# Performance work log

Measured on AMD Instinct MI355X. Metric: run time of the kernel, lower is better.

## Reference

```python
import jax, jax.numpy as jnp
import numpy as np

B, SQ, SKV, D, H = 4, 2048, 2048, 1024, 16
DH = D // H  # 64


def setup_inputs() -> dict:
    key = jax.random.key(0)
    ks = jax.random.split(key, 8)
    s = 0.02  # realistic init scale for weights
    return {
        "query": jax.random.normal(ks[0], (B, SQ, D), dtype=jnp.float32),
        "value": jax.random.normal(ks[1], (B, SKV, D), dtype=jnp.float32),
        "wq": jax.random.normal(ks[2], (H, D, DH), dtype=jnp.float32) * s,
        "bq": jnp.zeros((H, DH), dtype=jnp.float32),
        "wk": jax.random.normal(ks[3], (H, D, DH), dtype=jnp.float32) * s,
        "bk": jnp.zeros((H, DH), dtype=jnp.float32),
        "wv": jax.random.normal(ks[4], (H, D, DH), dtype=jnp.float32) * s,
        "bv": jnp.zeros((H, DH), dtype=jnp.float32),
        "wo": jax.random.normal(ks[5], (D, D), dtype=jnp.float32) * s,
        "bo": jnp.zeros((D,), dtype=jnp.float32),
    }


def reference(query, value, wq, bq, wk, bk, wv, bv, wo, bo):
    # Batched equivalent of the per-head Dense loop: [B,S,D] x [H,D,DH] -> [B,H,S,DH]
    q = jnp.einsum("bsd,hde->bhse", query, wq) + bq[None, :, None, :]
    k = jnp.einsum("bsd,hde->bhse", value, wk) + bk[None, :, None, :]
    v = jnp.einsum("bsd,hde->bhse", value, wv) + bv[None, :, None, :]
    scale = 1.0 / jnp.sqrt(jnp.asarray(DH, dtype=q.dtype))
    scores = jnp.einsum("bhqe,bhke->bhqk", q, k) * scale  # [B,H,SQ,SKV]
    align = jax.nn.softmax(scores, axis=-1)
    heads = jnp.einsum("bhqk,bhke->bhqe", align, v)  # [B,H,SQ,DH]
    # concat heads along feature dim (head order preserved)
    heads = jnp.transpose(heads, (0, 2, 1, 3)).reshape(B, SQ, D)
    return heads @ wo + bo
```

## Files before the change

### kernel.cpp

```cpp
#include <hip/hip_runtime.h>
#include <stdint.h>

#define DEVI __device__ __forceinline__

typedef __bf16  bf16x8 __attribute__((ext_vector_type(8)));
typedef float   f32x4  __attribute__((ext_vector_type(4)));
typedef float   f32x16 __attribute__((ext_vector_type(16)));
typedef uint32_t u32x4 __attribute__((ext_vector_type(4)));
typedef uint32_t u32x2v __attribute__((ext_vector_type(2)));
typedef uint16_t u16x8 __attribute__((ext_vector_type(8)));
typedef uint16_t u16x4 __attribute__((ext_vector_type(4)));

static constexpr int BB = 4, SQL = 2048, SKVL = 2048, DMODEL = 1024, NH = 16;
static constexpr int MROWS = BB * SQL;
static constexpr int KD = DMODEL;

DEVI uint16_t f2bf(float x) {
  uint32_t u = __builtin_bit_cast(uint32_t, x);
  u += 0x7FFFu + ((u >> 16) & 1u);
  return (uint16_t)(u >> 16);
}
DEVI uint32_t cvt2bf(float a, float b) {
  __bf16 x = (__bf16)a, y = (__bf16)b;
  return (uint32_t)__builtin_bit_cast(uint16_t, x) |
         ((uint32_t)__builtin_bit_cast(uint16_t, y) << 16);
}
DEVI f32x4 mfma16(bf16x8 a, bf16x8 b, f32x4 c) {
  return __builtin_amdgcn_mfma_f32_16x16x32_bf16(a, b, c, 0, 0, 0);
}
DEVI f32x16 mfma32(bf16x8 a, bf16x8 b, f32x16 c) {
  return __builtin_amdgcn_mfma_f32_32x32x16_bf16(a, b, c, 0, 0, 0);
}
DEVI void gload16(const void* g, void* l) {
  __builtin_amdgcn_global_load_lds((__attribute__((address_space(1))) const void*)g,
                                   (__attribute__((address_space(3))) void*)l, 16, 0, 0);
}
DEVI bf16x8 ldread(const void* p) { return __builtin_bit_cast(bf16x8, *(const u32x4*)p); }
DEVI u32x2v plswap(uint32_t a, uint32_t b) {
  return __builtin_amdgcn_permlane32_swap(a, b, false, false);
}

__global__ __launch_bounds__(256) void k_cvt_act(const float* __restrict__ q, const float* __restrict__ v,
                                                 uint16_t* __restrict__ aq, uint16_t* __restrict__ av) {
  const int64_t n4 = (int64_t)MROWS * DMODEL / 4;
  for (int64_t i = (int64_t)blockIdx.x * 256 + threadIdx.x; i < 2 * n4; i += (int64_t)gridDim.x * 256) {
    const bool second = (i >= n4);
    const int64_t j = second ? i - n4 : i;
    const float4 x = (second ? (const float4*)v : (const float4*)q)[j];
    u16x4 o = { f2bf(x.x), f2bf(x.y), f2bf(x.z), f2bf(x.w) };
    *(u16x4*)((second ? av : aq) + j * 4) = o;
  }
}

__global__ __launch_bounds__(256) void k_cvt_w(const float* __restrict__ wq, const float* __restrict__ wk,
                                               const float* __restrict__ wv, const float* __restrict__ wo,
                                               uint16_t* __restrict__ wt) {
  const int idx = blockIdx.x * 256 + threadIdx.x;
  const int z = idx >> 20, f = idx & 1048575;
  const int n = f >> 10, d = f & 1023;
  const float* w = (z == 0) ? wq : (z == 1) ? wk : (z == 2) ? wv : wo;
  const float x = (z < 3) ? w[((n >> 6) << 16) + d * 64 + (n & 63)] : w[d * 1024 + n];
  wt[(size_t)z * 1048576 + f] = f2bf(x);
}

template <int MODE>
__global__ __launch_bounds__(256) void k_gemm(const uint16_t* __restrict__ A, const uint16_t* __restrict__ Bt,
                                              const float* __restrict__ bias, const float* __restrict__ biasB,
                                              void* __restrict__ outp, void* __restrict__ outpB,
                                              float oscale) {
  __shared__ __align__(16) uint16_t Al[128 * 64];
  __shared__ __align__(16) uint16_t Bl[128 * 64];
  const int tid = threadIdx.x;
  const int w = tid >> 6, ln = tid & 63;
  const int g = ln >> 4, lc = ln & 15;
  const int m0 = blockIdx.x * 128, n0 = blockIdx.y * 128;
  const int wm = (w >> 1) * 64, wn = (w & 1) * 64;
  const int srow = w * 32 + (ln >> 3);
  const int colp = (ln & 7) * 16;

  f32x4 acc[4][4] = {};

  for (int kt = 0; kt < KD / 64; ++kt) {
    #pragma unroll
    for (int i = 0; i < 4; ++i) {
      const int row = srow + i * 8;
      const int colb = colp ^ ((row & 7) << 4);
      gload16((const char*)(A + (size_t)(m0 + row) * KD + kt * 64) + colb,
              (char*)Al + w * 4096 + i * 1024);
      gload16((const char*)(Bt + (size_t)(n0 + row) * KD + kt * 64) + colb,
              (char*)Bl + w * 4096 + i * 1024);
    }
    __syncthreads();
    #pragma unroll
    for (int kk = 0; kk < 2; ++kk) {
      bf16x8 af[4], bfr[4];
      #pragma unroll
      for (int mt = 0; mt < 4; ++mt) {
        const int row = wm + mt * 16 + lc;
        af[mt] = ldread((const char*)Al + row * 128 + ((kk * 64 + g * 16) ^ ((row & 7) << 4)));
      }
      #pragma unroll
      for (int nt = 0; nt < 4; ++nt) {
        const int row = wn + nt * 16 + lc;
        bfr[nt] = ldread((const char*)Bl + row * 128 + ((kk * 64 + g * 16) ^ ((row & 7) << 4)));
      }
      #pragma unroll
      for (int mt = 0; mt < 4; ++mt)
        #pragma unroll
        for (int nt = 0; nt < 4; ++nt)
          acc[mt][nt] = mfma16(af[mt], bfr[nt], acc[mt][nt]);
    }
    __syncthreads();
  }
  #pragma unroll
  for (int nt = 0; nt < 4; ++nt) {
    const int n = n0 + wn + nt * 16 + lc;
    const int z = (MODE == 2) ? (n >> 10) : 0;
    const int nn = (MODE == 2) ? (n & 1023) : n;
    const float bv = (MODE == 2) ? (z ? biasB : bias)[nn] : bias[n];
    uint16_t* dst16 = (uint16_t*)((MODE == 2 && z) ? outpB : outp);
    #pragma unroll
    for (int mt = 0; mt < 4; ++mt) {
      #pragma unroll
      for (int r = 0; r < 4; ++r) {
        const int m = m0 + wm + mt * 16 + g * 4 + r;
        if (MODE != 1) {
          float val = acc[mt][nt][r] + bv;
          if (MODE == 0) val *= oscale;
          const int b = m >> 11, s = m & 2047, h = nn >> 6, e = nn & 63;
          dst16[((size_t)((b * NH + h) * SQL + s)) * 64 + e] = f2bf(val);
        } else {
          ((float*)outp)[(size_t)m * DMODEL + n] = acc[mt][nt][r] + bv;
        }
      }
    }
  }
}

__global__ __launch_bounds__(512, 4) void k_attn(const uint16_t* __restrict__ Qb,
                                                 const uint16_t* __restrict__ Kb,
                                                 const uint16_t* __restrict__ Vb,
                                                 uint16_t* __restrict__ Hd) {
  __shared__ __align__(16) uint16_t Kl[2][64 * 64];
  __shared__ __align__(16) uint16_t Vl[2][64 * 64];
  const int tid = threadIdx.x;
  const int w = tid >> 6, ln = tid & 63;
  const int ql = ln & 31, hi = ln >> 5;
  const int bh = blockIdx.y;
  const int q0 = blockIdx.x * 256 + w * 32;

  const uint16_t* Qp = Qb + ((size_t)bh * SQL + q0 + ql) * 64;
  bf16x8 qf[4];
  #pragma unroll
  for (int s = 0; s < 4; ++s)
    qf[s] = __builtin_bit_cast(bf16x8, *(const u16x8*)(Qp + s * 16 + hi * 8));

  const uint16_t* Kbase = Kb + (size_t)bh * SKVL * 64;
  const uint16_t* Vbase = Vb + (size_t)bh * SKVL * 64;

  const int swl = (ln & 7) << 4;
  const int e0off = (hi << 4) ^ swl;
  const int rb = ql * 128;

  const bool kstage = (w < 4);
  const int krow0 = (w & 3) * 16 + (ln >> 3);
  const int kcolb = (((ln & 7) ^ (ln >> 3)) << 4);
  const int t2 = tid & 255;
  const int vkv = (t2 & 31) * 2, ve0 = (t2 >> 5) * 8;

  f32x16 acc0 = {}, acc1 = {};
  float lsum = 0.f;

  if (kstage) {
    #pragma unroll
    for (int i = 0; i < 2; ++i) {
      const int row = krow0 + i * 8;
      gload16((const char*)(Kbase + (size_t)row * 64) + kcolb,
              (char*)&Kl[0][0] + (w & 3) * 2048 + i * 1024);
    }
  } else {
    const u16x8 a = *(const u16x8*)(Vbase + (size_t)vkv * 64 + ve0);
    const u16x8 b = *(const u16x8*)(Vbase + (size_t)(vkv + 1) * 64 + ve0);
    #pragma unroll
    for (int i = 0; i < 8; ++i) {
      const int e = ve0 + i;
      *(uint32_t*)((char*)&Vl[0][0] + e * 128 + ((vkv * 2) ^ ((e & 7) << 4))) =
          (uint32_t)a[i] | ((uint32_t)b[i] << 16);
    }
  }
  __syncthreads();

  int cur = 0;
  for (int t = 0; t < SKVL / 64; ++t) {
    const bool pre = (t + 1 < SKVL / 64);
    u16x8 nv0, nv1;
    if (pre) {
      if (kstage) {
        const uint16_t* Kc = Kbase + (size_t)(t + 1) * 4096;
        #pragma unroll
        for (int i = 0; i < 2; ++i) {
          const int row = krow0 + i * 8;
          gload16((const char*)(Kc + (size_t)row * 64) + kcolb,
                  (char*)&Kl[cur ^ 1][0] + (w & 3) * 2048 + i * 1024);
        }
      } else {
        const uint16_t* Vc = Vbase + (size_t)(t + 1) * 4096;
        nv0 = *(const u16x8*)(Vc + (size_t)vkv * 64 + ve0);
        nv1 = *(const u16x8*)(Vc + (size_t)(vkv + 1) * 64 + ve0);
      }
    }
    const char* Kc0 = (const char*)&Kl[cur][0];
    f32x16 s0 = {}, s1 = {};
    __builtin_amdgcn_s_setprio(1);
    #pragma unroll
    for (int s = 0; s < 4; ++s) {
      const int off = e0off ^ (s << 5);
      const bf16x8 k0 = ldread(Kc0 + rb + off);
      const bf16x8 k1 = ldread(Kc0 + 4096 + rb + off);
      s0 = mfma32(k0, qf[s], s0);
      s1 = mfma32(k1, qf[s], s1);
    }
    __builtin_amdgcn_s_setprio(0);
    float ps = 0.f;
    #pragma unroll
    for (int r = 0; r < 16; ++r) {
      s0[r] = __builtin_amdgcn_exp2f(s0[r]);
      s1[r] = __builtin_amdgcn_exp2f(s1[r]);
      ps += s0[r] + s1[r];
    }
    lsum += ps;
    uint32_t w32[2][4][2];
    #pragma unroll
    for (int c8 = 0; c8 < 4; ++c8) {
      #pragma unroll
      for (int p = 0; p < 2; ++p) {
        w32[0][c8][p] = cvt2bf(s0[4 * c8 + 2 * p], s0[4 * c8 + 2 * p + 1]);
        w32[1][c8][p] = cvt2bf(s1[4 * c8 + 2 * p], s1[4 * c8 + 2 * p + 1]);
      }
    }
    const char* Vc0 = (const char*)&Vl[cur][0];
    __builtin_amdgcn_s_setprio(1);
    #pragma unroll
    for (int u = 0; u < 4; ++u) {
      const int tt = u >> 1, ul = u & 1;
      const u32x2v e0 = plswap(w32[tt][2 * ul][0], w32[tt][2 * ul + 1][0]);
      const u32x2v e1 = plswap(w32[tt][2 * ul][1], w32[tt][2 * ul + 1][1]);
      u32x4 pj;
      pj[0] = e0[0]; pj[1] = e1[0]; pj[2] = e0[1]; pj[3] = e1[1];
      const bf16x8 pb = __builtin_bit_cast(bf16x8, pj);
      const int off = e0off ^ (u << 5);
      const bf16x8 v0 = ldread(Vc0 + rb + off);
      const bf16x8 v1 = ldread(Vc0 + 4096 + rb + off);
      acc0 = mfma32(v0, pb, acc0);
      acc1 = mfma32(v1, pb, acc1);
    }
    __builtin_amdgcn_s_setprio(0);
    if (pre && !kstage) {
      #pragma unroll
      for (int i = 0; i < 8; ++i) {
        const int e = ve0 + i;
        *(uint32_t*)((char*)&Vl[cur ^ 1][0] + e * 128 + ((vkv * 2) ^ ((e & 7) << 4))) =
            (uint32_t)nv0[i] | ((uint32_t)nv1[i] << 16);
      }
    }
    __syncthreads();
    cur ^= 1;
  }
  const float lt = lsum + __shfl_xor(lsum, 32);
  const float inv = __builtin_amdgcn_rcpf(lt);
  const int b = bh >> 4, h = bh & 15;
  uint16_t* op = Hd + ((size_t)(b * SQL + q0 + ql)) * DMODEL + h * 64;
  #pragma unroll
  for (int et = 0; et < 2; ++et) {
    #pragma unroll
    for (int r2 = 0; r2 < 8; ++r2) {
      const float v0 = (et ? acc1[2 * r2] : acc0[2 * r2]) * inv;
      const float v1 = (et ? acc1[2 * r2 + 1] : acc0[2 * r2 + 1]) * inv;
      const int e = et * 32 + 4 * hi + (r2 & 1) * 2 + (r2 >> 1) * 8;
      *(uint32_t*)(op + e) = cvt2bf(v0, v1);
    }
  }
}

extern "C" void kernel_launch(void* const* d_in, const int* in_sizes, int n_in,
                              void* d_out, int out_size, void* d_ws, size_t ws_size,
                              hipStream_t stream) {
  const float* query = (const float*)d_in[0];
  const float* value = (const float*)d_in[1];
  const float* wq = (const float*)d_in[2];
  const float* bq = (const float*)d_in[3];
  const float* wk = (const float*)d_in[4];
  const float* bk = (const float*)d_in[5];
  const float* wv = (const float*)d_in[6];
  const float* bv = (const float*)d_in[7];
  const float* wo = (const float*)d_in[8];
  const float* bo = (const float*)d_in[9];

  const size_t SZ_ACT = (size_t)MROWS * DMODEL * 2;
  const size_t SZ_W   = (size_t)4 * DMODEL * DMODEL * 2;
  if (ws_size < 6 * SZ_ACT + SZ_W) return;

  char* ws = (char*)d_ws;
  uint16_t* Aq = (uint16_t*)ws;  ws += SZ_ACT;
  uint16_t* Av = (uint16_t*)ws;  ws += SZ_ACT;
  uint16_t* Wt = (uint16_t*)ws;  ws += SZ_W;
  uint16_t* Qb = (uint16_t*)ws;  ws += SZ_ACT;
  uint16_t* Kb = (uint16_t*)ws;  ws += SZ_ACT;
  uint16_t* Vb = (uint16_t*)ws;  ws += SZ_ACT;
  uint16_t* Hd = (uint16_t*)ws;  ws += SZ_ACT;

  const float QSCALE = 0.18033688011112042f;

  k_cvt_act<<<dim3(2048), dim3(256), 0, stream>>>(query, value, Aq, Av);
  k_cvt_w<<<dim3(16384), dim3(256), 0, stream>>>(wq, wk, wv, wo, Wt);
  k_gemm<0><<<dim3(64, 8), dim3(256), 0, stream>>>(Aq, Wt, bq, nullptr, Qb, nullptr, QSCALE);
  k_gemm<2><<<dim3(64, 16), dim3(256), 0, stream>>>(Av, Wt + 1048576, bk, bv, Kb, Vb, 1.0f);
  k_attn<<<dim3(8, 64), dim3(512), 0, stream>>>(Qb, Kb, Vb, Hd);
  k_gemm<1><<<dim3(64, 8), dim3(256), 0, stream>>>(Hd, Wt + 3145728, bo, nullptr, d_out, nullptr, 1.0f);
}
```

Measured before the change: 219.8 us.

## Double-buffer GEMM LDS, fuse conversion kernels, reshape attention blocks with XCD swizzle

Merges the activation and weight bf16 conversion kernels into a single launch. Adds LDS double buffering to the GEMM so the next K tile loads while MFMAs run on the current one, with one barrier per iteration instead of two. Reshapes the attention kernel from 512-thread blocks with specialised K and V loader warps into 256-thread blocks where every warp stages both K and V. It also remaps the 1D grid so consecutive blocks spread across XCDs. The GEMM doubles its LDS use and the attention change alters occupancy and per-warp load work.

```diff
diff --git a/kernel.cpp b/kernel.cpp
--- a/kernel.cpp
+++ b/kernel.cpp
@@ -40,27 +40,29 @@
   return __builtin_amdgcn_permlane32_swap(a, b, false, false);
 }
 
-__global__ __launch_bounds__(256) void k_cvt_act(const float* __restrict__ q, const float* __restrict__ v,
-                                                 uint16_t* __restrict__ aq, uint16_t* __restrict__ av) {
-  const int64_t n4 = (int64_t)MROWS * DMODEL / 4;
-  for (int64_t i = (int64_t)blockIdx.x * 256 + threadIdx.x; i < 2 * n4; i += (int64_t)gridDim.x * 256) {
-    const bool second = (i >= n4);
-    const int64_t j = second ? i - n4 : i;
-    const float4 x = (second ? (const float4*)v : (const float4*)q)[j];
-    u16x4 o = { f2bf(x.x), f2bf(x.y), f2bf(x.z), f2bf(x.w) };
-    *(u16x4*)((second ? av : aq) + j * 4) = o;
-  }
-}
-
-__global__ __launch_bounds__(256) void k_cvt_w(const float* __restrict__ wq, const float* __restrict__ wk,
-                                               const float* __restrict__ wv, const float* __restrict__ wo,
-                                               uint16_t* __restrict__ wt) {
-  const int idx = blockIdx.x * 256 + threadIdx.x;
-  const int z = idx >> 20, f = idx & 1048575;
-  const int n = f >> 10, d = f & 1023;
-  const float* w = (z == 0) ? wq : (z == 1) ? wk : (z == 2) ? wv : wo;
-  const float x = (z < 3) ? w[((n >> 6) << 16) + d * 64 + (n & 63)] : w[d * 1024 + n];
-  wt[(size_t)z * 1048576 + f] = f2bf(x);
+__global__ __launch_bounds__(256) void k_cvt(const float* __restrict__ q, const float* __restrict__ v,
+                                             const float* __restrict__ wq, const float* __restrict__ wk,
+                                             const float* __restrict__ wv, const float* __restrict__ wo,
+                                             uint16_t* __restrict__ aq, uint16_t* __restrict__ av,
+                                             uint16_t* __restrict__ wt) {
+  const int bx = blockIdx.x;
+  if (bx < 16384) {
+    const int idx = bx * 256 + threadIdx.x;
+    const int z = idx >> 20, f = idx & 1048575;
+    const int n = f >> 10, d = f & 1023;
+    const float* w = (z == 0) ? wq : (z == 1) ? wk : (z == 2) ? wv : wo;
+    const float x = (z < 3) ? w[((n >> 6) << 16) + d * 64 + (n & 63)] : w[d * 1024 + n];
+    wt[(size_t)z * 1048576 + f] = f2bf(x);
+  } else {
+    const int64_t n4 = (int64_t)MROWS * DMODEL / 4;
+    for (int64_t i = (int64_t)(bx - 16384) * 256 + threadIdx.x; i < 2 * n4; i += (int64_t)2048 * 256) {
+      const bool second = (i >= n4);
+      const int64_t j = second ? i - n4 : i;
+      const float4 x = (second ? (const float4*)v : (const float4*)q)[j];
+      u16x4 o = { f2bf(x.x), f2bf(x.y), f2bf(x.z), f2bf(x.w) };
+      *(u16x4*)((second ? av : aq) + j * 4) = o;
+    }
+  }
 }
 
 template <int MODE>
@@ -68,8 +70,8 @@
                                               const float* __restrict__ bias, const float* __restrict__ biasB,
                                               void* __restrict__ outp, void* __restrict__ outpB,
                                               float oscale) {
-  __shared__ __align__(16) uint16_t Al[128 * 64];
-  __shared__ __align__(16) uint16_t Bl[128 * 64];
+  __shared__ __align__(16) uint16_t Al[2][128 * 64];
+  __shared__ __align__(16) uint16_t Bl[2][128 * 64];
   const int tid = threadIdx.x;
   const int w = tid >> 6, ln = tid & 63;
   const int g = ln >> 4, lc = ln & 15;
@@ -80,29 +82,41 @@
 
   f32x4 acc[4][4] = {};
 
-  for (int kt = 0; kt < KD / 64; ++kt) {
+  auto stage = [&](int kt, int bs) {
     #pragma unroll
     for (int i = 0; i < 4; ++i) {
       const int row = srow + i * 8;
       const int colb = colp ^ ((row & 7) << 4);
       gload16((const char*)(A + (size_t)(m0 + row) * KD + kt * 64) + colb,
-              (char*)Al + w * 4096 + i * 1024);
+              (char*)&Al[bs][0] + w * 4096 + i * 1024);
       gload16((const char*)(Bt + (size_t)(n0 + row) * KD + kt * 64) + colb,
-              (char*)Bl + w * 4096 + i * 1024);
-    }
-    __syncthreads();
+              (char*)&Bl[bs][0] + w * 4096 + i * 1024);
+    }
+  };
+
+  stage(0, 0);
+  asm volatile("s_waitcnt vmcnt(0)" ::: "memory");
+  __builtin_amdgcn_s_barrier();
+  __builtin_amdgcn_sched_barrier(0);
+
+  int cur = 0;
+  #pragma unroll 2
+  for (int kt = 0; kt < KD / 64; ++kt) {
+    if (kt + 1 < KD / 64) stage(kt + 1, cur ^ 1);
+    const char* Ac = (const char*)&Al[cur][0];
+    const char* Bc = (const char*)&Bl[cur][0];
     #pragma unroll
     for (int kk = 0; kk < 2; ++kk) {
       bf16x8 af[4], bfr[4];
       #pragma unroll
       for (int mt = 0; mt < 4; ++mt) {
         const int row = wm + mt * 16 + lc;
-        af[mt] = ldread((const char*)Al + row * 128 + ((kk * 64 + g * 16) ^ ((row & 7) << 4)));
+        af[mt] = ldread(Ac + row * 128 + ((kk * 64 + g * 16) ^ ((row & 7) << 4)));
       }
       #pragma unroll
       for (int nt = 0; nt < 4; ++nt) {
         const int row = wn + nt * 16 + lc;
-        bfr[nt] = ldread((const char*)Bl + row * 128 + ((kk * 64 + g * 16) ^ ((row & 7) << 4)));
+        bfr[nt] = ldread(Bc + row * 128 + ((kk * 64 + g * 16) ^ ((row & 7) << 4)));
       }
       #pragma unroll
       for (int mt = 0; mt < 4; ++mt)
@@ -110,8 +124,12 @@
         for (int nt = 0; nt < 4; ++nt)
           acc[mt][nt] = mfma16(af[mt], bfr[nt], acc[mt][nt]);
     }
-    __syncthreads();
-  }
+    asm volatile("s_waitcnt vmcnt(0)" ::: "memory");
+    __builtin_amdgcn_s_barrier();
+    __builtin_amdgcn_sched_barrier(0);
+    cur ^= 1;
+  }
+
   #pragma unroll
   for (int nt = 0; nt < 4; ++nt) {
     const int n = n0 + wn + nt * 16 + lc;
@@ -137,7 +155,7 @@
   }
 }
 
-__global__ __launch_bounds__(512, 4) void k_attn(const uint16_t* __restrict__ Qb,
+__global__ __launch_bounds__(256, 3) void k_attn(const uint16_t* __restrict__ Qb,
                                                  const uint16_t* __restrict__ Kb,
                                                  const uint16_t* __restrict__ Vb,
                                                  uint16_t* __restrict__ Hd) {
@@ -146,8 +164,10 @@
   const int tid = threadIdx.x;
   const int w = tid >> 6, ln = tid & 63;
   const int ql = ln & 31, hi = ln >> 5;
-  const int bh = blockIdx.y;
-  const int q0 = blockIdx.x * 256 + w * 32;
+  const int bsw = blockIdx.x;
+  const int l = (bsw & 7) * 128 + (bsw >> 3);
+  const int qx = l & 15, bh = l >> 4;
+  const int q0 = qx * 128 + w * 32;
 
   const uint16_t* Qp = Qb + ((size_t)bh * SQL + q0 + ql) * 64;
   bf16x8 qf[4];
@@ -162,23 +182,20 @@
   const int e0off = (hi << 4) ^ swl;
   const int rb = ql * 128;
 
-  const bool kstage = (w < 4);
-  const int krow0 = (w & 3) * 16 + (ln >> 3);
+  const int krow0 = w * 16 + (ln >> 3);
   const int kcolb = (((ln & 7) ^ (ln >> 3)) << 4);
-  const int t2 = tid & 255;
-  const int vkv = (t2 & 31) * 2, ve0 = (t2 >> 5) * 8;
+  const int vkv = (tid & 31) * 2, ve0 = (tid >> 5) * 8;
 
   f32x16 acc0 = {}, acc1 = {};
   float lsum = 0.f;
 
-  if (kstage) {
+  {
     #pragma unroll
     for (int i = 0; i < 2; ++i) {
       const int row = krow0 + i * 8;
       gload16((const char*)(Kbase + (size_t)row * 64) + kcolb,
-              (char*)&Kl[0][0] + (w & 3) * 2048 + i * 1024);
-    }
-  } else {
+              (char*)&Kl[0][0] + w * 2048 + i * 1024);
+    }
     const u16x8 a = *(const u16x8*)(Vbase + (size_t)vkv * 64 + ve0);
     const u16x8 b = *(const u16x8*)(Vbase + (size_t)(vkv + 1) * 64 + ve0);
     #pragma unroll
@@ -195,19 +212,16 @@
     const bool pre = (t + 1 < SKVL / 64);
     u16x8 nv0, nv1;
     if (pre) {
-      if (kstage) {
-        const uint16_t* Kc = Kbase + (size_t)(t + 1) * 4096;
-        #pragma unroll
-        for (int i = 0; i < 2; ++i) {
-          const int row = krow0 + i * 8;
-          gload16((const char*)(Kc + (size_t)row * 64) + kcolb,
-                  (char*)&Kl[cur ^ 1][0] + (w & 3) * 2048 + i * 1024);
-        }
-      } else {
-        const uint16_t* Vc = Vbase + (size_t)(t + 1) * 4096;
-        nv0 = *(const u16x8*)(Vc + (size_t)vkv * 64 + ve0);
-        nv1 = *(const u16x8*)(Vc + (size_t)(vkv + 1) * 64 + ve0);
-      }
+      const uint16_t* Kc = Kbase + (size_t)(t + 1) * 4096;
+      #pragma unroll
+      for (int i = 0; i < 2; ++i) {
+        const int row = krow0 + i * 8;
+        gload16((const char*)(Kc + (size_t)row * 64) + kcolb,
+                (char*)&Kl[cur ^ 1][0] + w * 2048 + i * 1024);
+      }
+      const uint16_t* Vc = Vbase + (size_t)(t + 1) * 4096;
+      nv0 = *(const u16x8*)(Vc + (size_t)vkv * 64 + ve0);
+      nv1 = *(const u16x8*)(Vc + (size_t)(vkv + 1) * 64 + ve0);
     }
     const char* Kc0 = (const char*)&Kl[cur][0];
     f32x16 s0 = {}, s1 = {};
@@ -255,7 +269,7 @@
       acc1 = mfma32(v1, pb, acc1);
     }
     __builtin_amdgcn_s_setprio(0);
-    if (pre && !kstage) {
+    if (pre) {
       #pragma unroll
       for (int i = 0; i < 8; ++i) {
         const int e = ve0 + i;
@@ -266,18 +280,20 @@
     __syncthreads();
     cur ^= 1;
   }
-  const float lt = lsum + __shfl_xor(lsum, 32);
-  const float inv = __builtin_amdgcn_rcpf(lt);
-  const int b = bh >> 4, h = bh & 15;
-  uint16_t* op = Hd + ((size_t)(b * SQL + q0 + ql)) * DMODEL + h * 64;
-  #pragma unroll
-  for (int et = 0; et < 2; ++et) {
-    #pragma unroll
-    for (int r2 = 0; r2 < 8; ++r2) {
-      const float v0 = (et ? acc1[2 * r2] : acc0[2 * r2]) * inv;
-      const float v1 = (et ? acc1[2 * r2 + 1] : acc0[2 * r2 + 1]) * inv;
-      const int e = et * 32 + 4 * hi + (r2 & 1) * 2 + (r2 >> 1) * 8;
-      *(uint32_t*)(op + e) = cvt2bf(v0, v1);
+  {
+    const float lt = lsum + __shfl_xor(lsum, 32);
+    const float inv = __builtin_amdgcn_rcpf(lt);
+    const int b = bh >> 4, h = bh & 15;
+    uint16_t* op = Hd + ((size_t)(b * SQL + q0 + ql)) * DMODEL + h * 64;
+    #pragma unroll
+    for (int et = 0; et < 2; ++et) {
+      #pragma unroll
+      for (int r2 = 0; r2 < 8; ++r2) {
+        const float v0 = (et ? acc1[2 * r2] : acc0[2 * r2]) * inv;
+        const float v1 = (et ? acc1[2 * r2 + 1] : acc0[2 * r2 + 1]) * inv;
+        const int e = et * 32 + 4 * hi + (r2 & 1) * 2 + (r2 >> 1) * 8;
+        *(uint32_t*)(op + e) = cvt2bf(v0, v1);
+      }
     }
   }
 }
@@ -311,10 +327,9 @@
 
   const float QSCALE = 0.18033688011112042f;
 
-  k_cvt_act<<<dim3(2048), dim3(256), 0, stream>>>(query, value, Aq, Av);
-  k_cvt_w<<<dim3(16384), dim3(256), 0, stream>>>(wq, wk, wv, wo, Wt);
+  k_cvt<<<dim3(18432), dim3(256), 0, stream>>>(query, value, wq, wk, wv, wo, Aq, Av, Wt);
   k_gemm<0><<<dim3(64, 8), dim3(256), 0, stream>>>(Aq, Wt, bq, nullptr, Qb, nullptr, QSCALE);
   k_gemm<2><<<dim3(64, 16), dim3(256), 0, stream>>>(Av, Wt + 1048576, bk, bv, Kb, Vb, 1.0f);
-  k_attn<<<dim3(8, 64), dim3(512), 0, stream>>>(Qb, Kb, Vb, Hd);
+  k_attn<<<dim3(1024), dim3(256), 0, stream>>>(Qb, Kb, Vb, Hd);
   k_gemm<1><<<dim3(64, 8), dim3(256), 0, stream>>>(Hd, Wt + 3145728, bo, nullptr, d_out, nullptr, 1.0f);
 }
```

After: 229.7 us. 4.5% more time.
